# Kernel optimization log

Hardware: AMD Instinct MI355X
Metric: run time of the kernel (lower is better)

## Reference

```python
import jax, jax.numpy as jnp
import numpy as np

IN_SIZE = 256
OUT_SIZE = 2


def setup_inputs() -> dict:
    key = jax.random.key(0)
    k1, k2, k3, k4 = jax.random.split(key, 4)
    B, S, D, O = 32, 1024, IN_SIZE, OUT_SIZE
    input1 = jax.random.normal(k1, (B, S, D), dtype=jnp.float32)
    input2 = jax.random.normal(k2, (B, S, D), dtype=jnp.float32)
    # learned parameters
    w1 = jax.random.normal(k3, (D, O, D), dtype=jnp.float32) * 0.02
    w2 = jax.random.normal(k4, (2 * D + 1, O), dtype=jnp.float32) * 0.02
    return {"input1": input1, "input2": input2, "w1": w1, "w2": w2}


def reference(input1, input2, w1, w2):
    D = w1.shape[0]
    # bilinear term: bxi,ioj,byj -> bxyo
    logits1 = jnp.einsum('bxi,ioj,byj->bxyo', input1, w1, input2)
    # linear term: original concat([f1, f2, 1]) @ w2 == input1 @ w2[:D]
    # broadcast over y, plus input2 @ w2[D:2D] broadcast over x, plus bias w2[2D]
    lin1 = jnp.einsum('bxd,do->bxo', input1, w2[:D])        # (B, S, O)
    lin2 = jnp.einsum('byd,do->byo', input2, w2[D:2 * D])   # (B, S, O)
    bias = w2[2 * D]                                        # (O,)
    logits2 = lin1[:, :, None, :] + lin2[:, None, :, :] + bias
    return logits1 + logits2
```

## Files before the change

### kernel.cpp

```cpp
#include <hip/hip_runtime.h>
#include <hip/hip_bf16.h>
#include <cstdint>
#include <cstddef>


typedef __bf16 bf16_t;
typedef __bf16 bf16x4 __attribute__((ext_vector_type(4)));
typedef __bf16 bf16x8 __attribute__((ext_vector_type(8)));
typedef float  f32x4  __attribute__((ext_vector_type(4)));

#define NB   32
#define NS   1024
#define ND   256
#define NM   (NB * NS)
#define NN1  512

__device__ __forceinline__ void gload_lds16(const void* g, void* l) {
  __builtin_amdgcn_global_load_lds(
      (__attribute__((address_space(1))) void*)g,
      (__attribute__((address_space(3))) void*)l, 16, 0, 0);
}

__global__ __launch_bounds__(256) void prep_kernel(
    const float* __restrict__ in1, const float* __restrict__ in2,
    const float* __restrict__ w1,  const float* __restrict__ w2,
    bf16_t* __restrict__ in1b, bf16_t* __restrict__ in2b,
    bf16_t* __restrict__ w1t,  float* __restrict__ lin)
{
  int bid = blockIdx.x;
  if (bid < 16384) {
    int wave = threadIdx.x >> 6;
    int lane = threadIdx.x & 63;
    int r  = bid * 4 + wave;
    int is2 = (r >= NM) ? 1 : 0;
    int lr = r & (NM - 1);
    const float* src = is2 ? in2 : in1;
    bf16_t*      dst = is2 ? in2b : in1b;

    float4 v = *(const float4*)(src + (size_t)lr * ND + lane * 4);
    bf16x4 h;
    h[0] = (bf16_t)v.x; h[1] = (bf16_t)v.y; h[2] = (bf16_t)v.z; h[3] = (bf16_t)v.w;
    *(bf16x4*)(dst + (size_t)lr * ND + lane * 4) = h;

    int dbase = is2 * ND + lane * 4;
    float a0 = v.x * w2[(dbase + 0) * 2 + 0] + v.y * w2[(dbase + 1) * 2 + 0]
             + v.z * w2[(dbase + 2) * 2 + 0] + v.w * w2[(dbase + 3) * 2 + 0];
    float a1 = v.x * w2[(dbase + 0) * 2 + 1] + v.y * w2[(dbase + 1) * 2 + 1]
             + v.z * w2[(dbase + 2) * 2 + 1] + v.w * w2[(dbase + 3) * 2 + 1];
    #pragma unroll
    for (int off = 32; off > 0; off >>= 1) {
      a0 += __shfl_down(a0, off, 64);
      a1 += __shfl_down(a1, off, 64);
    }
    if (lane == 0) {
      if (is2) { a0 += w2[2 * ND * 2 + 0]; a1 += w2[2 * ND * 2 + 1]; }
      lin[r * 2 + 0] = a0;
      lin[r * 2 + 1] = a1;
    }
  } else {
    int wb = bid - 16384;
    int t  = threadIdx.x;
    #pragma unroll
    for (int e = 0; e < 8; ++e) {
      int q  = wb * 2048 + e * 256 + t;
      int oj = q >> 8;
      int i  = q & 255;
      w1t[q] = (bf16_t)w1[i * NN1 + oj];
    }
  }
}

__global__ __launch_bounds__(256, 3) void gemm1_kernel(
    const bf16_t* __restrict__ A, const bf16_t* __restrict__ Bt,
    bf16_t* __restrict__ T)
{
  __shared__ __align__(16) bf16_t Ap[64 * 256];
  __shared__ __align__(16) bf16_t Bc[2][128 * 32];

  int m0 = blockIdx.x * 64;
  int t = threadIdx.x, lane = t & 63, wid = t >> 6;
  int wm = (wid >> 1) * 32, wn = (wid & 1) * 64;

  #pragma unroll
  for (int i = 0; i < 8; ++i) {
    int unit = i * 256 + t;
    int row = unit >> 5;
    int c   = unit & 31;
    int cs  = c ^ (row & 7);
    gload_lds16(A + (size_t)(m0 + row) * ND + cs * 8, (char*)Ap + unit * 16);
  }
  #pragma unroll
  for (int i = 0; i < 2; ++i) {
    int unit = i * 256 + t;
    int row = unit >> 2, c = unit & 3, cs = c ^ (row & 3);
    gload_lds16(Bt + (size_t)row * ND + cs * 8, (char*)Bc[0] + unit * 16);
  }
  __syncthreads();

  f32x4 acc[2][4] = {};

  for (int s = 0; s < 32; ++s) {
    if (s + 1 < 32) {
      int nt = (s + 1) >> 3, j0 = ((s + 1) & 7) * 32;
      bf16_t* dst = (bf16_t*)Bc[(s + 1) & 1];
      #pragma unroll
      for (int i = 0; i < 2; ++i) {
        int unit = i * 256 + t;
        int row = unit >> 2, c = unit & 3, cs = c ^ (row & 3);
        gload_lds16(Bt + (size_t)(nt * 128 + row) * ND + j0 + cs * 8,
                    (char*)dst + unit * 16);
      }
    }
    const bf16_t* Bcur = Bc[s & 1];
    bf16x8 bfr[4];
    #pragma unroll
    for (int ni = 0; ni < 4; ++ni) {
      int r = wn + ni * 16 + (lane & 15);
      int cp = (lane >> 4) ^ (r & 3);
      bfr[ni] = *(const bf16x8*)&Bcur[r * 32 + cp * 8];
    }
    #pragma unroll
    for (int mi = 0; mi < 2; ++mi) {
      int r = wm + mi * 16 + (lane & 15);
      int cl = (s & 7) * 4 + (lane >> 4);
      int cp = cl ^ (r & 7);
      bf16x8 af = *(const bf16x8*)&Ap[r * 256 + cp * 8];
      #pragma unroll
      for (int ni = 0; ni < 4; ++ni)
        acc[mi][ni] = __builtin_amdgcn_mfma_f32_16x16x32_bf16(
            af, bfr[ni], acc[mi][ni], 0, 0, 0);
    }
    if ((s & 7) == 7) {
      int nt = s >> 3;
      #pragma unroll
      for (int mi = 0; mi < 2; ++mi) {
        int row = m0 + wm + mi * 16 + ((lane >> 4) << 2);
        #pragma unroll
        for (int ni = 0; ni < 4; ++ni) {
          int col = nt * 128 + wn + ni * 16 + (lane & 15);
          #pragma unroll
          for (int r_ = 0; r_ < 4; ++r_)
            T[(size_t)(row + r_) * NN1 + col] = (bf16_t)acc[mi][ni][r_];
          acc[mi][ni] = (f32x4){0.f, 0.f, 0.f, 0.f};
        }
      }
    }
    __syncthreads();
  }
}

__global__ __launch_bounds__(256, 2) void gemm2_kernel(
    const bf16_t* __restrict__ Tm, const bf16_t* __restrict__ in2b,
    const float* __restrict__ lin, float* __restrict__ out)
{
  __shared__ __align__(16) bf16_t Ap[64 * 512];
  __shared__ __align__(16) bf16_t Bc[2][64 * 32];

  int blk = (blockIdx.x & 7) * 64 + (blockIdx.x >> 3);
  int b   = blk >> 4;
  int x0  = (blk & 15) * 64;
  const bf16_t* Tb = Tm   + (size_t)b * NS * NN1;
  const bf16_t* Ib = in2b + (size_t)b * NS * ND;

  int t = threadIdx.x, lane = t & 63, wid = t >> 6;
  int wm = (wid >> 1) * 32, wn = (wid & 1) * 32;

  #pragma unroll
  for (int i = 0; i < 16; ++i) {
    int unit = i * 256 + t;
    int row = unit >> 6;
    int c   = unit & 63;
    int cs  = c ^ (row & 7);
    gload_lds16(Tb + (size_t)(x0 + row) * NN1 + cs * 8, (char*)Ap + unit * 16);
  }
  {
    int row = t >> 2, c = t & 3, cs = c ^ (row & 3);
    gload_lds16(Ib + (size_t)row * ND + cs * 8, (char*)Bc[0] + t * 16);
  }
  __syncthreads();

  f32x4 acc0[2][2] = {};
  f32x4 acc1[2][2] = {};
  float2* outb = (float2*)(out + (size_t)b * NS * NS * 2);
  const float2* l1p = (const float2*)(lin + (size_t)b * NS * 2);
  const float2* l2p = (const float2*)(lin + (size_t)(NM + b * NS) * 2);

  for (int s = 0; s < 128; ++s) {
    if (s + 1 < 128) {
      int yi = (s + 1) >> 3, j0 = ((s + 1) & 7) * 32;
      bf16_t* dst = (bf16_t*)Bc[(s + 1) & 1];
      int row = t >> 2, c = t & 3, cs = c ^ (row & 3);
      gload_lds16(Ib + (size_t)(yi * 64 + row) * ND + j0 + cs * 8,
                  (char*)dst + t * 16);
    }
    const bf16_t* Bcur = Bc[s & 1];
    bf16x8 bfr[2];
    #pragma unroll
    for (int ni = 0; ni < 2; ++ni) {
      int r = wn + ni * 16 + (lane & 15);
      int cp = (lane >> 4) ^ (r & 3);
      bfr[ni] = *(const bf16x8*)&Bcur[r * 32 + cp * 8];
    }
    #pragma unroll
    for (int mi = 0; mi < 2; ++mi) {
      int r = wm + mi * 16 + (lane & 15);
      int cl = (s & 7) * 4 + (lane >> 4);
      int cp0 = cl ^ (r & 7);
      bf16x8 af0 = *(const bf16x8*)&Ap[r * 512 + cp0 * 8];
      #pragma unroll
      for (int ni = 0; ni < 2; ++ni)
        acc0[mi][ni] = __builtin_amdgcn_mfma_f32_16x16x32_bf16(
            af0, bfr[ni], acc0[mi][ni], 0, 0, 0);
      int cp1 = (cl + 32) ^ (r & 7);
      bf16x8 af1 = *(const bf16x8*)&Ap[r * 512 + cp1 * 8];
      #pragma unroll
      for (int ni = 0; ni < 2; ++ni)
        acc1[mi][ni] = __builtin_amdgcn_mfma_f32_16x16x32_bf16(
            af1, bfr[ni], acc1[mi][ni], 0, 0, 0);
    }
    if ((s & 7) == 7) {
      int y0 = (s >> 3) * 64;
      #pragma unroll
      for (int mi = 0; mi < 2; ++mi) {
        int rb = x0 + wm + mi * 16 + ((lane >> 4) << 2);
        float2 l1[4];
        #pragma unroll
        for (int r_ = 0; r_ < 4; ++r_) l1[r_] = l1p[rb + r_];
        #pragma unroll
        for (int ni = 0; ni < 2; ++ni) {
          int col = y0 + wn + ni * 16 + (lane & 15);
          float2 l2 = l2p[col];
          #pragma unroll
          for (int r_ = 0; r_ < 4; ++r_) {
            float2 v;
            v.x = acc0[mi][ni][r_] + l1[r_].x + l2.x;
            v.y = acc1[mi][ni][r_] + l1[r_].y + l2.y;
            outb[(size_t)(rb + r_) * NS + col] = v;
          }
          acc0[mi][ni] = (f32x4){0.f, 0.f, 0.f, 0.f};
          acc1[mi][ni] = (f32x4){0.f, 0.f, 0.f, 0.f};
        }
      }
    }
    __syncthreads();
  }
}

extern "C" void kernel_launch(void* const* d_in, const int* in_sizes, int n_in,
                              void* d_out, int out_size, void* d_ws, size_t ws_size,
                              hipStream_t stream) {
  const float* in1 = (const float*)d_in[0];
  const float* in2 = (const float*)d_in[1];
  const float* w1  = (const float*)d_in[2];
  const float* w2  = (const float*)d_in[3];
  float* out = (float*)d_out;

  char* ws = (char*)d_ws;
  bf16_t* in1b = (bf16_t*)(ws);
  bf16_t* in2b = (bf16_t*)(ws + (16u << 20));
  bf16_t* w1t  = (bf16_t*)(ws + (32u << 20));
  float*  lin  = (float*) (ws + (32u << 20) + (256u << 10));
  bf16_t* T    = (bf16_t*)(ws + (33u << 20));

  prep_kernel<<<16448, 256, 0, stream>>>(in1, in2, w1, w2, in1b, in2b, w1t, lin);
  gemm1_kernel<<<512, 256, 0, stream>>>(in1b, w1t, T);
  gemm2_kernel<<<512, 256, 0, stream>>>(T, in2b, lin, out);
}
```

Baseline: 133.9 us.

## Hold A operands in registers and switch gemm2 to 32x32 MFMA tiles

```diff
diff --git a/kernel.cpp b/kernel.cpp
--- a/kernel.cpp
+++ b/kernel.cpp
@@ -8,6 +8,7 @@
 typedef __bf16 bf16x4 __attribute__((ext_vector_type(4)));
 typedef __bf16 bf16x8 __attribute__((ext_vector_type(8)));
 typedef float  f32x4  __attribute__((ext_vector_type(4)));
+typedef float  f32x16 __attribute__((ext_vector_type(16)));
 
 #define NB   32
 #define NS   1024
@@ -153,8 +154,9 @@
     const bf16_t* __restrict__ Tm, const bf16_t* __restrict__ in2b,
     const float* __restrict__ lin, float* __restrict__ out)
 {
-  __shared__ __align__(16) bf16_t Ap[64 * 512];
-  __shared__ __align__(16) bf16_t Bc[2][64 * 32];
+  __shared__ __align__(16) char smem[65536];
+  bf16_t* Ap = (bf16_t*)smem;
+  bf16_t* Bbuf[2] = { (bf16_t*)smem, (bf16_t*)(smem + 16384) };
 
   int blk = (blockIdx.x & 7) * 64 + (blockIdx.x >> 3);
   int b   = blk >> 4;
@@ -163,7 +165,9 @@
   const bf16_t* Ib = in2b + (size_t)b * NS * ND;
 
   int t = threadIdx.x, lane = t & 63, wid = t >> 6;
-  int wm = (wid >> 1) * 32, wn = (wid & 1) * 32;
+  int wx = (wid >> 1) * 32;
+  int wy = (wid & 1) * 64;
+  int l31 = lane & 31, lhi = lane >> 5;
 
   #pragma unroll
   for (int i = 0; i < 16; ++i) {
@@ -173,76 +177,91 @@
     int cs  = c ^ (row & 7);
     gload_lds16(Tb + (size_t)(x0 + row) * NN1 + cs * 8, (char*)Ap + unit * 16);
   }
+  __syncthreads();
+
+  bf16x8 af[2][16];
   {
-    int row = t >> 2, c = t & 3, cs = c ^ (row & 3);
-    gload_lds16(Ib + (size_t)row * ND + cs * 8, (char*)Bc[0] + t * 16);
-  }
-  __syncthreads();
-
-  f32x4 acc0[2][2] = {};
-  f32x4 acc1[2][2] = {};
+    int row = wx + l31;
+    #pragma unroll
+    for (int o = 0; o < 2; ++o)
+      #pragma unroll
+      for (int ks = 0; ks < 16; ++ks) {
+        int ls = o * 32 + ks * 2 + lhi;
+        int sm = ls ^ (row & 7);
+        af[o][ks] = *(const bf16x8*)&Ap[(row * 64 + sm) * 8];
+      }
+  }
+  __syncthreads();
+
+  #pragma unroll
+  for (int i = 0; i < 4; ++i) {
+    int u = i * 256 + t;
+    int row = u >> 3, sm = u & 7;
+    int cs = sm ^ (row & 7);
+    gload_lds16(Ib + (size_t)row * ND + cs * 8, (char*)Bbuf[0] + u * 16);
+  }
+  __syncthreads();
+
+  f32x16 acc[2][2] = {};
   float2* outb = (float2*)(out + (size_t)b * NS * NS * 2);
   const float2* l1p = (const float2*)(lin + (size_t)b * NS * 2);
   const float2* l2p = (const float2*)(lin + (size_t)(NM + b * NS) * 2);
 
-  for (int s = 0; s < 128; ++s) {
-    if (s + 1 < 128) {
-      int yi = (s + 1) >> 3, j0 = ((s + 1) & 7) * 32;
-      bf16_t* dst = (bf16_t*)Bc[(s + 1) & 1];
-      int row = t >> 2, c = t & 3, cs = c ^ (row & 3);
-      gload_lds16(Ib + (size_t)(yi * 64 + row) * ND + j0 + cs * 8,
-                  (char*)dst + t * 16);
-    }
-    const bf16_t* Bcur = Bc[s & 1];
-    bf16x8 bfr[2];
-    #pragma unroll
-    for (int ni = 0; ni < 2; ++ni) {
-      int r = wn + ni * 16 + (lane & 15);
-      int cp = (lane >> 4) ^ (r & 3);
-      bfr[ni] = *(const bf16x8*)&Bcur[r * 32 + cp * 8];
-    }
-    #pragma unroll
-    for (int mi = 0; mi < 2; ++mi) {
-      int r = wm + mi * 16 + (lane & 15);
-      int cl = (s & 7) * 4 + (lane >> 4);
-      int cp0 = cl ^ (r & 7);
-      bf16x8 af0 = *(const bf16x8*)&Ap[r * 512 + cp0 * 8];
-      #pragma unroll
-      for (int ni = 0; ni < 2; ++ni)
-        acc0[mi][ni] = __builtin_amdgcn_mfma_f32_16x16x32_bf16(
-            af0, bfr[ni], acc0[mi][ni], 0, 0, 0);
-      int cp1 = (cl + 32) ^ (r & 7);
-      bf16x8 af1 = *(const bf16x8*)&Ap[r * 512 + cp1 * 8];
-      #pragma unroll
-      for (int ni = 0; ni < 2; ++ni)
-        acc1[mi][ni] = __builtin_amdgcn_mfma_f32_16x16x32_bf16(
-            af1, bfr[ni], acc1[mi][ni], 0, 0, 0);
-    }
-    if ((s & 7) == 7) {
-      int y0 = (s >> 3) * 64;
-      #pragma unroll
-      for (int mi = 0; mi < 2; ++mi) {
-        int rb = x0 + wm + mi * 16 + ((lane >> 4) << 2);
-        float2 l1[4];
-        #pragma unroll
-        for (int r_ = 0; r_ < 4; ++r_) l1[r_] = l1p[rb + r_];
-        #pragma unroll
-        for (int ni = 0; ni < 2; ++ni) {
-          int col = y0 + wn + ni * 16 + (lane & 15);
-          float2 l2 = l2p[col];
+  for (int yi = 0; yi < 8; ++yi) {
+    #pragma unroll
+    for (int kc = 0; kc < 4; ++kc) {
+      if (yi < 7 || kc < 3) {
+        int c1 = yi * 4 + kc + 1;
+        int yn = c1 >> 2, kn = (c1 & 3) * 64;
+        char* dst = (char*)Bbuf[(kc + 1) & 1];
+        #pragma unroll
+        for (int i = 0; i < 4; ++i) {
+          int u = i * 256 + t;
+          int row = u >> 3, sm = u & 7;
+          int cs = sm ^ (row & 7);
+          gload_lds16(Ib + (size_t)(yn * 128 + row) * ND + kn + cs * 8,
+                      dst + u * 16);
+        }
+      }
+      const bf16_t* Bp = Bbuf[kc & 1];
+      #pragma unroll
+      for (int ni = 0; ni < 2; ++ni) {
+        int row = wy + ni * 32 + l31;
+        #pragma unroll
+        for (int k2 = 0; k2 < 4; ++k2) {
+          int ls = k2 * 2 + lhi;
+          int sm = ls ^ (row & 7);
+          bf16x8 bf = *(const bf16x8*)&Bp[(row * 8 + sm) * 8];
+          acc[ni][0] = __builtin_amdgcn_mfma_f32_32x32x16_bf16(
+              af[0][kc * 4 + k2], bf, acc[ni][0], 0, 0, 0);
+          acc[ni][1] = __builtin_amdgcn_mfma_f32_32x32x16_bf16(
+              af[1][kc * 4 + k2], bf, acc[ni][1], 0, 0, 0);
+        }
+      }
+      if (kc == 3) {
+        int y0 = yi * 128;
+        float2 l2[2];
+        #pragma unroll
+        for (int ni = 0; ni < 2; ++ni) l2[ni] = l2p[y0 + wy + ni * 32 + l31];
+        int xr = x0 + wx + 4 * lhi;
+        #pragma unroll
+        for (int r = 0; r < 16; ++r) {
+          int row = xr + (r & 3) + 8 * (r >> 2);
+          float2 l1 = l1p[row];
           #pragma unroll
-          for (int r_ = 0; r_ < 4; ++r_) {
+          for (int ni = 0; ni < 2; ++ni) {
+            int col = y0 + wy + ni * 32 + l31;
             float2 v;
-            v.x = acc0[mi][ni][r_] + l1[r_].x + l2.x;
-            v.y = acc1[mi][ni][r_] + l1[r_].y + l2.y;
-            outb[(size_t)(rb + r_) * NS + col] = v;
+            v.x = acc[ni][0][r] + l1.x + l2[ni].x;
+            v.y = acc[ni][1][r] + l1.y + l2[ni].y;
+            outb[(size_t)row * NS + col] = v;
           }
-          acc0[mi][ni] = (f32x4){0.f, 0.f, 0.f, 0.f};
-          acc1[mi][ni] = (f32x4){0.f, 0.f, 0.f, 0.f};
-        }
-      }
-    }
-    __syncthreads();
+        }
+        acc[0][0] = (f32x16)(0.f); acc[0][1] = (f32x16)(0.f);
+        acc[1][0] = (f32x16)(0.f); acc[1][1] = (f32x16)(0.f);
+      }
+      __syncthreads();
+    }
   }
 }
 
```

Result: faster. 118.3 us, median of 2 (-11.6%).
